# Optimization experiments

Measured on AMD Instinct MI355X. Metric: run time of the kernel, lower is better.

The kernel has to match this reference:

```python
import jax, jax.numpy as jnp
import numpy as np

N_E = 8192      # codebook size
E_DIM = 256     # codebook dim
BETA = 0.25

def setup_inputs() -> dict:
    key = jax.random.key(0)
    k1, k2 = jax.random.split(key)
    z = jax.random.normal(k1, (4, E_DIM, 16, 16, 16), dtype=jnp.float32)
    weight = jax.random.normal(k2, (N_E, E_DIM), dtype=jnp.float32)
    return {"z": z, "weight": weight}

def reference(z, weight):
    # b c d h w -> b d h w c
    z_t = jnp.transpose(z, (0, 2, 3, 4, 1))
    zf = z_t.reshape(-1, E_DIM)                          # [N, e_dim]
    # l2 pairwise distances: |z|^2 + |w|^2 - 2 z.w^T
    d = (jnp.sum(zf * zf, axis=1, keepdims=True)
         + jnp.sum(weight * weight, axis=1)
         - 2.0 * jnp.einsum('bd,nd->bn', zf, weight))    # [N, n_e]
    idx = jnp.argmin(d, axis=1)                          # [N]
    z_q = weight[idx].reshape(z_t.shape)                 # gather lookup
    # perplexity from cluster assignment histogram (avoids dense one-hot)
    counts = jax.ops.segment_sum(jnp.ones_like(idx, dtype=z.dtype), idx,
                                 num_segments=N_E)
    avg_probs = counts / zf.shape[0]
    perplexity = jnp.exp(-jnp.sum(avg_probs * jnp.log(avg_probs + 1e-10)))
    # commitment loss (z_q detached)
    loss = BETA * jnp.mean((jax.lax.stop_gradient(z_q) - z_t) ** 2)
    # straight-through estimator
    z_q_st = z_t + jax.lax.stop_gradient(z_q - z_t)
    out = jnp.transpose(z_q_st, (0, 4, 1, 2, 3))         # b d h w c -> b c d h w
    return out, loss, perplexity, idx
```

## Files before the change

kernel.cpp:

```cpp
#include <hip/hip_runtime.h>
#include <stdint.h>


#define M_TOTAL 16384
#define N_CODES 8192
#define KDIM    256
#define SPATIAL 4096
#define NSPLIT  8
#define CODES_PER_SPLIT  1024
#define CHUNK_CODES      16
#define CHUNKS_PER_SPLIT 64
#define CHUNK_BYTES      9216
#define CHUNK_HALFS      4608

typedef _Float16 v8hf __attribute__((ext_vector_type(8)));
typedef _Float16 v4hf __attribute__((ext_vector_type(4)));
typedef float    v4f  __attribute__((ext_vector_type(4)));

#define WAITCNT_VM9   0x0F79
#define WAITCNT_VM0   0x0F70
#define WAITCNT_LGKM0 0xC07F

__global__ __launch_bounds__(256) void prep_w_kernel(
    const float* __restrict__ w, _Float16* __restrict__ wpk,
    int* __restrict__ counts, double* __restrict__ loss_acc)
{
    const int t = threadIdx.x;
    const int n = blockIdx.x * 4 + (t >> 6);
    const int lane = t & 63;
    v4f v = ((const v4f*)(w + (size_t)n * KDIM))[lane];
    v4hf hv;
    float s = 0.0f;
#pragma unroll
    for (int j = 0; j < 4; j++) {
        float f = v[j];
        s += f * f;
        hv[j] = (_Float16)f;
    }
    const int chunk = n >> 4;
    const int row   = n & 15;
    const int g     = lane >> 1;
    const int gg    = g ^ (n & 7);
    size_t off = (size_t)chunk * CHUNK_HALFS + row * 256 + gg * 8 + (lane & 1) * 4;
    *(v4hf*)(wpk + off) = hv;
#pragma unroll
    for (int o = 32; o >= 1; o >>= 1) s += __shfl_xor(s, o);
    if (lane == 0) {
        float* hwp = (float*)((char*)wpk + (size_t)chunk * CHUNK_BYTES + 8192);
        hwp[row] = 1024.0f - 0.5f * s;
    }
    const int gi = blockIdx.x * 256 + t;
    if (gi < N_CODES) counts[gi] = 0;
    if (gi == 0) *loss_acc = 0.0;
}

__device__ __forceinline__ void top2max_merge(uint32_t& v1, int& i1, uint32_t& v2, int& i2,
                                              uint32_t o1, int oi1, uint32_t o2, int oi2) {
    bool ob = (o1 > v1) || (o1 == v1 && oi1 < i1);
    uint32_t n1v, n2v; int n1i, n2i;
    if (ob) {
        bool t2 = (v1 > o2) || (v1 == o2 && i1 < oi2);
        n1v = o1; n1i = oi1;
        n2v = t2 ? v1 : o2; n2i = t2 ? i1 : oi2;
    } else {
        bool t2 = (o1 > v2) || (o1 == v2 && oi1 < i2);
        n1v = v1; n1i = i1;
        n2v = t2 ? o1 : v2; n2i = t2 ? oi1 : i2;
    }
    v1 = n1v; i1 = n1i; v2 = n2v; i2 = n2i;
}

__global__ __launch_bounds__(64, 2) void gemm_kernel(
    const float* __restrict__ z,
    const _Float16* __restrict__ wpk,
    int4* __restrict__ candbuf)
{
    __shared__ __align__(16) _Float16 lds[2][CHUNK_HALFS];

    const int bid   = blockIdx.x;
    const int split = bid & 7;
    const int rb    = bid >> 3;
    const int i0    = rb * 64;
    const int b     = i0 >> 12;
    const int s0    = i0 & (SPATIAL - 1);
    const int lane  = threadIdx.x;
    const int r     = lane & 15;
    const int q     = lane >> 4;

    const char* wsplit = (const char*)wpk + (size_t)split * CHUNKS_PER_SPLIT * CHUNK_BYTES;
    auto stage = [&](int chunk, int buf) {
        const char* gb = wsplit + (size_t)chunk * CHUNK_BYTES + lane * 16;
        _Float16* lb = &lds[buf][lane * 8];
#pragma unroll
        for (int j = 0; j < 9; j++) {
            __builtin_amdgcn_global_load_lds(
                (const __attribute__((address_space(1))) void*)(gb + j * 1024),
                (__attribute__((address_space(3))) void*)(lb + j * 512), 16, 0, 0);
        }
    };
    stage(0, 0);
    stage(1, 1);

    v8hf a[4][8];
    {
        const float* zb = z + ((size_t)b << 20) + (size_t)(s0 + r);
#pragma unroll
        for (int mt = 0; mt < 4; mt++) {
#pragma unroll
            for (int ks = 0; ks < 8; ks++) {
                const int kbase = ks * 32 + q * 8;
#pragma unroll
                for (int j = 0; j < 8; j++)
                    a[mt][ks][j] = (_Float16)zb[((size_t)(kbase + j) << 12) + mt * 16];
            }
        }
    }

    uint32_t k1[4][4], k2[4][4];
#pragma unroll
    for (int mt = 0; mt < 4; mt++)
#pragma unroll
    for (int g = 0; g < 4; g++) { k1[mt][g] = 0u; k2[mt][g] = 0u; }

    const int swz = r & 7;

    auto body = [&](int it, int buf) {
        const float hwv = *(const float*)((const char*)&lds[buf][0] + 8192 + r * 4);
        v4f acc[4];
#pragma unroll
        for (int mt = 0; mt < 4; mt++) acc[mt] = (v4f){hwv, hwv, hwv, hwv};

        const _Float16* L = &lds[buf][0];
#pragma unroll
        for (int ks = 0; ks < 8; ks++) {
            const int gran = ((ks << 2) | q) ^ swz;
            v8hf bh = *(const v8hf*)(L + r * 256 + (gran << 3));
#pragma unroll
            for (int mt = 0; mt < 4; mt++)
                acc[mt] = __builtin_amdgcn_mfma_f32_16x16x32_f16(a[mt][ks], bh, acc[mt], 0, 0, 0);
        }
        const uint32_t tag = (uint32_t)it;
#pragma unroll
        for (int mt = 0; mt < 4; mt++)
#pragma unroll
        for (int g = 0; g < 4; g++) {
            uint32_t key = (__float_as_uint(acc[mt][g]) & 0xFFFFFFC0u) | tag;
            uint32_t o1 = k1[mt][g], o2 = k2[mt][g];
            uint32_t hi = key > o2 ? key : o2;
            k2[mt][g] = hi < o1 ? hi : o1;
            k1[mt][g] = key > o1 ? key : o1;
        }
    };

#pragma unroll 1
    for (int it = 0; it < CHUNKS_PER_SPLIT - 1; it++) {
        const int buf = it & 1;
        __builtin_amdgcn_s_waitcnt(WAITCNT_VM9);
        body(it, buf);
        __builtin_amdgcn_s_waitcnt(WAITCNT_LGKM0);
        if (it < CHUNKS_PER_SPLIT - 2) stage(it + 2, buf);
    }
    __builtin_amdgcn_s_waitcnt(WAITCNT_VM0);
    body(CHUNKS_PER_SPLIT - 1, (CHUNKS_PER_SPLIT - 1) & 1);

    const int nsbase = split * CODES_PER_SPLIT + r;
#pragma unroll
    for (int mt = 0; mt < 4; mt++) {
#pragma unroll
        for (int g = 0; g < 4; g++) {
            uint32_t K1 = k1[mt][g], K2 = k2[mt][g];
            int n1 = nsbase + (int)((K1 & 63u) << 4);
            int n2 = nsbase + (int)((K2 & 63u) << 4);
#pragma unroll
            for (int off = 1; off < 16; off <<= 1) {
                uint32_t o1 = __shfl_xor(K1, off);
                int     on1 = __shfl_xor(n1, off);
                uint32_t o2 = __shfl_xor(K2, off);
                int     on2 = __shfl_xor(n2, off);
                top2max_merge(K1, n1, K2, n2, o1, on1, o2, on2);
            }
            if (r == 0) {
                const int row = i0 + mt * 16 + q * 4 + g;
                candbuf[(size_t)row * 8 + split] = make_int4((int)K1, n1, (int)K2, n2);
            }
        }
    }
}

__global__ __launch_bounds__(256) void finish_kernel(
    const float* __restrict__ z, const float* __restrict__ weight,
    const int4* __restrict__ candbuf,
    int* __restrict__ counts, double* __restrict__ loss_acc,
    float* __restrict__ out, float* __restrict__ out_idx_f)
{
    __shared__ int4  s_cand[32][8];
    __shared__ float s_zw[32][KDIM + 1];
    __shared__ int   s_fi[32];
    __shared__ double s_loss[4];

    const int i0 = blockIdx.x * 32;
    const int b  = i0 >> 12;
    const int s0 = i0 & (SPATIAL - 1);
    const int t  = threadIdx.x;

    s_cand[t >> 3][t & 7] = candbuf[(size_t)(i0 + (t >> 3)) * 8 + (t & 7)];

    for (int e = t; e < 32 * KDIM; e += 256) {
        const int c = e >> 5, rr = e & 31;
        s_zw[rr][c] = z[((size_t)b << 20) + ((size_t)c << 12) + s0 + rr];
    }
    __syncthreads();

    const int row = t >> 3, seg = t & 7;
    float zs[32];
#pragma unroll
    for (int j = 0; j < 32; j++) zs[j] = s_zw[row][seg * 32 + j];

    float da[16];
    float dmin_a = 3.4e38f;
#pragma unroll
    for (int sp = 0; sp < 8; sp++) {
        int4 c = s_cand[row][sp];
        da[sp * 2]     = 2048.0f - 2.0f * __uint_as_float((uint32_t)c.x & 0xFFFFFFC0u);
        da[sp * 2 + 1] = 2048.0f - 2.0f * __uint_as_float((uint32_t)c.z & 0xFFFFFFC0u);
        dmin_a = fminf(dmin_a, fminf(da[sp * 2], da[sp * 2 + 1]));
    }
    const float cutoff = dmin_a + 0.5f;

    double dbest = 1e300; int nbest = 0x7fffffff;
#pragma unroll 1
    for (int c = 0; c < 16; c++) {
        if (da[c] > cutoff) continue;
        int4 cc = s_cand[row][c >> 1];
        const int n = (c & 1) ? cc.w : cc.y;
        const float* wr = weight + (size_t)n * KDIM + seg * 32;
        double d = 0.0;
#pragma unroll
        for (int j = 0; j < 32; j++) {
            double df = (double)zs[j] - (double)wr[j];
            d += df * df;
        }
#pragma unroll
        for (int o = 1; o < 8; o <<= 1) d += __shfl_xor(d, o);
        if (d < dbest || (d == dbest && n < nbest)) { dbest = d; nbest = n; }
    }

    double lsum = 0.0;
    if (seg == 0) {
        s_fi[row] = nbest;
        out_idx_f[i0 + row] = (float)nbest;
        atomicAdd(&counts[nbest], 1);
        lsum = dbest;
    }
#pragma unroll
    for (int o = 1; o < 64; o <<= 1) lsum += __shfl_xor(lsum, o);
    if ((t & 63) == 0) s_loss[t >> 6] = lsum;
    __syncthreads();
    if (t == 0) atomicAdd(loss_acc, s_loss[0] + s_loss[1] + s_loss[2] + s_loss[3]);

    for (int e = t; e < 32 * KDIM; e += 256) {
        const int rr = e >> 8, c = e & 255;
        s_zw[rr][c] = weight[(size_t)s_fi[rr] * KDIM + c];
    }
    __syncthreads();
    const int m = t & 31, c0 = t >> 5;
    const size_t obase = ((size_t)b << 20) + (size_t)(s0 + m);
    for (int c = c0; c < KDIM; c += 8)
        out[obase + ((size_t)c << 12)] = s_zw[m][c];
}

__global__ void finalize_kernel(const int* __restrict__ counts,
                                const double* __restrict__ loss_acc,
                                float* __restrict__ out_scalars)
{
    const int t = threadIdx.x;
    double s = 0.0;
    for (int n = t; n < N_CODES; n += 256) {
        double p = (double)counts[n] / (double)M_TOTAL;
        s -= p * log(p + 1e-10);
    }
#pragma unroll
    for (int o = 32; o >= 1; o >>= 1) s += __shfl_xor(s, o);
    __shared__ double sds[4];
    if ((t & 63) == 0) sds[t >> 6] = s;
    __syncthreads();
    if (t == 0) {
        double tot = sds[0] + sds[1] + sds[2] + sds[3];
        out_scalars[0] = (float)(0.25 * (*loss_acc) / (double)(M_TOTAL * KDIM));
        out_scalars[1] = (float)exp(tot);
    }
}

extern "C" void kernel_launch(void* const* d_in, const int* in_sizes, int n_in,
                              void* d_out, int out_size, void* d_ws, size_t ws_size,
                              hipStream_t stream) {
    const float* z      = (const float*)d_in[0];
    const float* weight = (const float*)d_in[1];
    float* out = (float*)d_out;

    size_t off = 0;
    auto carve = [&](size_t bytes) {
        void* p = (char*)d_ws + off;
        off += (bytes + 255) & ~(size_t)255;
        return p;
    };
    _Float16* wpk     = (_Float16*)carve((size_t)(N_CODES / CHUNK_CODES) * CHUNK_BYTES);
    int4*     candbuf = (int4*)    carve((size_t)M_TOTAL * 8 * 16);
    int*      counts  = (int*)     carve((size_t)N_CODES * 4);
    double*   lossac  = (double*)  carve(16);

    float* out_scalars = out + (size_t)4 * KDIM * SPATIAL;
    float* out_idx_f   = out_scalars + 2;

    prep_w_kernel<<<dim3(N_CODES / 4), dim3(256), 0, stream>>>(weight, wpk, counts, lossac);
    gemm_kernel<<<dim3(M_TOTAL / 64 * NSPLIT), dim3(64), 0, stream>>>(z, wpk, candbuf);
    finish_kernel<<<dim3(M_TOTAL / 32), dim3(256), 0, stream>>>(
        z, weight, candbuf, counts, lossac, out, out_idx_f);
    finalize_kernel<<<dim3(1), dim3(256), 0, stream>>>(counts, lossac, out_scalars);
}
```

Measured before the change: 209.8 us.

## Share codebook staging across four waves with 4-deep LDS ring and fuse finalize

The GEMM block grows from one wave to four, which share each 32-code fp16 codebook chunk staged in LDS through a 4-buffer ring with barriers. This cuts redundant global-to-LDS traffic per row. The |w|^2 bias now lives in a separate array that is preloaded into LDS. The single-block finalize kernel is folded into finish_kernel through a last-block-done atomic counter, which removes one launch but adds a serial tail in the last block. The grid drops to 512 blocks, so occupancy and latency hiding may change.

```diff
diff --git a/kernel.cpp b/kernel.cpp
--- a/kernel.cpp
+++ b/kernel.cpp
@@ -8,22 +8,19 @@
 #define SPATIAL 4096
 #define NSPLIT  8
 #define CODES_PER_SPLIT  1024
-#define CHUNK_CODES      16
-#define CHUNKS_PER_SPLIT 64
-#define CHUNK_BYTES      9216
-#define CHUNK_HALFS      4608
+#define CHUNK_CODES      32
+#define CHUNKS_PER_SPLIT 32
+#define CHUNK_HALFS      8192
+#define CHUNK_BYTES      16384
 
 typedef _Float16 v8hf __attribute__((ext_vector_type(8)));
 typedef _Float16 v4hf __attribute__((ext_vector_type(4)));
 typedef float    v4f  __attribute__((ext_vector_type(4)));
 
-#define WAITCNT_VM9   0x0F79
-#define WAITCNT_VM0   0x0F70
-#define WAITCNT_LGKM0 0xC07F
-
 __global__ __launch_bounds__(256) void prep_w_kernel(
     const float* __restrict__ w, _Float16* __restrict__ wpk,
-    int* __restrict__ counts, double* __restrict__ loss_acc)
+    float* __restrict__ hw_arr, int* __restrict__ counts,
+    double* __restrict__ loss_acc, int* __restrict__ done_ctr)
 {
     const int t = threadIdx.x;
     const int n = blockIdx.x * 4 + (t >> 6);
@@ -37,21 +34,17 @@
         s += f * f;
         hv[j] = (_Float16)f;
     }
-    const int chunk = n >> 4;
-    const int row   = n & 15;
-    const int g     = lane >> 1;
-    const int gg    = g ^ (n & 7);
+    const int chunk = n >> 5;
+    const int row   = n & 31;
+    const int gg    = (lane >> 1) ^ (n & 7);
     size_t off = (size_t)chunk * CHUNK_HALFS + row * 256 + gg * 8 + (lane & 1) * 4;
     *(v4hf*)(wpk + off) = hv;
 #pragma unroll
     for (int o = 32; o >= 1; o >>= 1) s += __shfl_xor(s, o);
-    if (lane == 0) {
-        float* hwp = (float*)((char*)wpk + (size_t)chunk * CHUNK_BYTES + 8192);
-        hwp[row] = 1024.0f - 0.5f * s;
-    }
+    if (lane == 0) hw_arr[n] = 1024.0f - 0.5f * s;
     const int gi = blockIdx.x * 256 + t;
     if (gi < N_CODES) counts[gi] = 0;
-    if (gi == 0) *loss_acc = 0.0;
+    if (gi == 0) { *loss_acc = 0.0; *done_ctr = 0; }
 }
 
 __device__ __forceinline__ void top2max_merge(uint32_t& v1, int& i1, uint32_t& v2, int& i2,
@@ -70,40 +63,48 @@
     v1 = n1v; i1 = n1i; v2 = n2v; i2 = n2i;
 }
 
-__global__ __launch_bounds__(64, 2) void gemm_kernel(
+__global__ __launch_bounds__(256, 2) void gemm_kernel(
     const float* __restrict__ z,
     const _Float16* __restrict__ wpk,
+    const float* __restrict__ hw_arr,
     int4* __restrict__ candbuf)
 {
-    __shared__ __align__(16) _Float16 lds[2][CHUNK_HALFS];
+    __shared__ __align__(16) _Float16 lds[4][CHUNK_HALFS];
+    __shared__ float hw_lds[CODES_PER_SPLIT];
 
     const int bid   = blockIdx.x;
     const int split = bid & 7;
     const int rb    = bid >> 3;
-    const int i0    = rb * 64;
+    const int i0    = rb * 256;
     const int b     = i0 >> 12;
     const int s0    = i0 & (SPATIAL - 1);
-    const int lane  = threadIdx.x;
+    const int tid   = threadIdx.x;
+    const int wave  = tid >> 6;
+    const int lane  = tid & 63;
     const int r     = lane & 15;
     const int q     = lane >> 4;
 
-    const char* wsplit = (const char*)wpk + (size_t)split * CHUNKS_PER_SPLIT * CHUNK_BYTES;
+    const char* wsplit = (const char*)wpk + (size_t)split * (CODES_PER_SPLIT * KDIM * 2);
     auto stage = [&](int chunk, int buf) {
-        const char* gb = wsplit + (size_t)chunk * CHUNK_BYTES + lane * 16;
-        _Float16* lb = &lds[buf][lane * 8];
-#pragma unroll
-        for (int j = 0; j < 9; j++) {
+        const char* gb = wsplit + (size_t)chunk * CHUNK_BYTES + tid * 16;
+        _Float16* lb = &lds[buf][tid * 8];
+#pragma unroll
+        for (int j = 0; j < 4; j++) {
             __builtin_amdgcn_global_load_lds(
-                (const __attribute__((address_space(1))) void*)(gb + j * 1024),
-                (__attribute__((address_space(3))) void*)(lb + j * 512), 16, 0, 0);
+                (const __attribute__((address_space(1))) void*)(gb + j * 4096),
+                (__attribute__((address_space(3))) void*)(lb + j * 2048), 16, 0, 0);
         }
     };
-    stage(0, 0);
-    stage(1, 1);
+    stage(0, 0); stage(1, 1); stage(2, 2);
+
+    {
+        v4f h = *(const v4f*)(hw_arr + split * CODES_PER_SPLIT + tid * 4);
+        *(v4f*)&hw_lds[tid * 4] = h;
+    }
 
     v8hf a[4][8];
     {
-        const float* zb = z + ((size_t)b << 20) + (size_t)(s0 + r);
+        const float* zb = z + ((size_t)b << 20) + (size_t)(s0 + wave * 64 + r);
 #pragma unroll
         for (int mt = 0; mt < 4; mt++) {
 #pragma unroll
@@ -124,44 +125,59 @@
 
     const int swz = r & 7;
 
+    __syncthreads();
+
     auto body = [&](int it, int buf) {
-        const float hwv = *(const float*)((const char*)&lds[buf][0] + 8192 + r * 4);
-        v4f acc[4];
-#pragma unroll
-        for (int mt = 0; mt < 4; mt++) acc[mt] = (v4f){hwv, hwv, hwv, hwv};
-
+        const float hw0 = hw_lds[it * 32 + r];
+        const float hw1 = hw_lds[it * 32 + 16 + r];
+        v4f acc[4][2];
+#pragma unroll
+        for (int mt = 0; mt < 4; mt++) {
+            acc[mt][0] = (v4f){hw0, hw0, hw0, hw0};
+            acc[mt][1] = (v4f){hw1, hw1, hw1, hw1};
+        }
         const _Float16* L = &lds[buf][0];
 #pragma unroll
-        for (int ks = 0; ks < 8; ks++) {
-            const int gran = ((ks << 2) | q) ^ swz;
-            v8hf bh = *(const v8hf*)(L + r * 256 + (gran << 3));
+        for (int st = 0; st < 2; st++) {
+            const int rowoff = (st * 16 + r) * 256;
+#pragma unroll
+            for (int ks = 0; ks < 8; ks++) {
+                const int gran = ((ks << 2) | q) ^ swz;
+                v8hf bh = *(const v8hf*)(L + rowoff + (gran << 3));
+#pragma unroll
+                for (int mt = 0; mt < 4; mt++)
+                    acc[mt][st] = __builtin_amdgcn_mfma_f32_16x16x32_f16(a[mt][ks], bh, acc[mt][st], 0, 0, 0);
+            }
+        }
+#pragma unroll
+        for (int st = 0; st < 2; st++) {
+            const uint32_t tag = (uint32_t)(it * 2 + st);
 #pragma unroll
             for (int mt = 0; mt < 4; mt++)
-                acc[mt] = __builtin_amdgcn_mfma_f32_16x16x32_f16(a[mt][ks], bh, acc[mt], 0, 0, 0);
-        }
-        const uint32_t tag = (uint32_t)it;
-#pragma unroll
-        for (int mt = 0; mt < 4; mt++)
-#pragma unroll
-        for (int g = 0; g < 4; g++) {
-            uint32_t key = (__float_as_uint(acc[mt][g]) & 0xFFFFFFC0u) | tag;
-            uint32_t o1 = k1[mt][g], o2 = k2[mt][g];
-            uint32_t hi = key > o2 ? key : o2;
-            k2[mt][g] = hi < o1 ? hi : o1;
-            k1[mt][g] = key > o1 ? key : o1;
+#pragma unroll
+            for (int g = 0; g < 4; g++) {
+                uint32_t key = (__float_as_uint(acc[mt][st][g]) & 0xFFFFFFC0u) | tag;
+                uint32_t o1 = k1[mt][g], o2 = k2[mt][g];
+                uint32_t hi = key > o2 ? key : o2;
+                k2[mt][g] = hi < o1 ? hi : o1;
+                k1[mt][g] = key > o1 ? key : o1;
+            }
         }
     };
 
 #pragma unroll 1
-    for (int it = 0; it < CHUNKS_PER_SPLIT - 1; it++) {
-        const int buf = it & 1;
-        __builtin_amdgcn_s_waitcnt(WAITCNT_VM9);
-        body(it, buf);
-        __builtin_amdgcn_s_waitcnt(WAITCNT_LGKM0);
-        if (it < CHUNKS_PER_SPLIT - 2) stage(it + 2, buf);
-    }
-    __builtin_amdgcn_s_waitcnt(WAITCNT_VM0);
-    body(CHUNKS_PER_SPLIT - 1, (CHUNKS_PER_SPLIT - 1) & 1);
+    for (int it = 0; it < CHUNKS_PER_SPLIT - 2; it++) {
+        asm volatile("s_waitcnt vmcnt(8)" ::: "memory");
+        asm volatile("s_barrier" ::: "memory");
+        if (it + 3 < CHUNKS_PER_SPLIT) stage(it + 3, (it + 3) & 3);
+        body(it, it & 3);
+    }
+    asm volatile("s_waitcnt vmcnt(4)" ::: "memory");
+    asm volatile("s_barrier" ::: "memory");
+    body(CHUNKS_PER_SPLIT - 2, (CHUNKS_PER_SPLIT - 2) & 3);
+    asm volatile("s_waitcnt vmcnt(0)" ::: "memory");
+    asm volatile("s_barrier" ::: "memory");
+    body(CHUNKS_PER_SPLIT - 1, (CHUNKS_PER_SPLIT - 1) & 3);
 
     const int nsbase = split * CODES_PER_SPLIT + r;
 #pragma unroll
@@ -180,7 +196,7 @@
                 top2max_merge(K1, n1, K2, n2, o1, on1, o2, on2);
             }
             if (r == 0) {
-                const int row = i0 + mt * 16 + q * 4 + g;
+                const int row = i0 + wave * 64 + mt * 16 + q * 4 + g;
                 candbuf[(size_t)row * 8 + split] = make_int4((int)K1, n1, (int)K2, n2);
             }
         }
@@ -191,12 +207,15 @@
     const float* __restrict__ z, const float* __restrict__ weight,
     const int4* __restrict__ candbuf,
     int* __restrict__ counts, double* __restrict__ loss_acc,
-    float* __restrict__ out, float* __restrict__ out_idx_f)
+    int* __restrict__ done_ctr,
+    float* __restrict__ out, float* __restrict__ out_scalars,
+    float* __restrict__ out_idx_f)
 {
     __shared__ int4  s_cand[32][8];
     __shared__ float s_zw[32][KDIM + 1];
     __shared__ int   s_fi[32];
-    __shared__ double s_loss[4];
+    __shared__ double s_red[4];
+    __shared__ int   s_last;
 
     const int i0 = blockIdx.x * 32;
     const int b  = i0 >> 12;
@@ -254,9 +273,9 @@
     }
 #pragma unroll
     for (int o = 1; o < 64; o <<= 1) lsum += __shfl_xor(lsum, o);
-    if ((t & 63) == 0) s_loss[t >> 6] = lsum;
-    __syncthreads();
-    if (t == 0) atomicAdd(loss_acc, s_loss[0] + s_loss[1] + s_loss[2] + s_loss[3]);
+    if ((t & 63) == 0) s_red[t >> 6] = lsum;
+    __syncthreads();
+    if (t == 0) atomicAdd(loss_acc, s_red[0] + s_red[1] + s_red[2] + s_red[3]);
 
     for (int e = t; e < 32 * KDIM; e += 256) {
         const int rr = e >> 8, c = e & 255;
@@ -267,27 +286,33 @@
     const size_t obase = ((size_t)b << 20) + (size_t)(s0 + m);
     for (int c = c0; c < KDIM; c += 8)
         out[obase + ((size_t)c << 12)] = s_zw[m][c];
-}
-
-__global__ void finalize_kernel(const int* __restrict__ counts,
-                                const double* __restrict__ loss_acc,
-                                float* __restrict__ out_scalars)
-{
-    const int t = threadIdx.x;
-    double s = 0.0;
-    for (int n = t; n < N_CODES; n += 256) {
-        double p = (double)counts[n] / (double)M_TOTAL;
-        s -= p * log(p + 1e-10);
-    }
-#pragma unroll
-    for (int o = 32; o >= 1; o >>= 1) s += __shfl_xor(s, o);
-    __shared__ double sds[4];
-    if ((t & 63) == 0) sds[t >> 6] = s;
-    __syncthreads();
+
     if (t == 0) {
-        double tot = sds[0] + sds[1] + sds[2] + sds[3];
-        out_scalars[0] = (float)(0.25 * (*loss_acc) / (double)(M_TOTAL * KDIM));
-        out_scalars[1] = (float)exp(tot);
+        __threadfence();
+        int old = __hip_atomic_fetch_add(done_ctr, 1, __ATOMIC_ACQ_REL,
+                                         __HIP_MEMORY_SCOPE_AGENT);
+        s_last = (old == (int)gridDim.x - 1);
+    }
+    __syncthreads();
+    if (s_last) {
+        double s = 0.0;
+        for (int n = t; n < N_CODES; n += 256) {
+            int c = __hip_atomic_load(&counts[n], __ATOMIC_RELAXED,
+                                      __HIP_MEMORY_SCOPE_AGENT);
+            double p = (double)c / (double)M_TOTAL;
+            s -= p * log(p + 1e-10);
+        }
+#pragma unroll
+        for (int o = 32; o >= 1; o >>= 1) s += __shfl_xor(s, o);
+        if ((t & 63) == 0) s_red[t >> 6] = s;
+        __syncthreads();
+        if (t == 0) {
+            double tot = s_red[0] + s_red[1] + s_red[2] + s_red[3];
+            double l = __hip_atomic_load(loss_acc, __ATOMIC_RELAXED,
+                                         __HIP_MEMORY_SCOPE_AGENT);
+            out_scalars[0] = (float)(0.25 * l / (double)(M_TOTAL * KDIM));
+            out_scalars[1] = (float)exp(tot);
+        }
     }
 }
 
@@ -304,17 +329,19 @@
         off += (bytes + 255) & ~(size_t)255;
         return p;
     };
-    _Float16* wpk     = (_Float16*)carve((size_t)(N_CODES / CHUNK_CODES) * CHUNK_BYTES);
+    _Float16* wpk     = (_Float16*)carve((size_t)N_CODES * KDIM * 2);
+    float*    hw_arr  = (float*)   carve((size_t)N_CODES * 4);
     int4*     candbuf = (int4*)    carve((size_t)M_TOTAL * 8 * 16);
     int*      counts  = (int*)     carve((size_t)N_CODES * 4);
     double*   lossac  = (double*)  carve(16);
+    int*      donec   = (int*)     carve(16);
 
     float* out_scalars = out + (size_t)4 * KDIM * SPATIAL;
     float* out_idx_f   = out_scalars + 2;
 
-    prep_w_kernel<<<dim3(N_CODES / 4), dim3(256), 0, stream>>>(weight, wpk, counts, lossac);
-    gemm_kernel<<<dim3(M_TOTAL / 64 * NSPLIT), dim3(64), 0, stream>>>(z, wpk, candbuf);
+    prep_w_kernel<<<dim3(N_CODES / 4), dim3(256), 0, stream>>>(
+        weight, wpk, hw_arr, counts, lossac, donec);
+    gemm_kernel<<<dim3(64 * NSPLIT), dim3(256), 0, stream>>>(z, wpk, hw_arr, candbuf);
     finish_kernel<<<dim3(M_TOTAL / 32), dim3(256), 0, stream>>>(
-        z, weight, candbuf, counts, lossac, out, out_idx_f);
-    finalize_kernel<<<dim3(1), dim3(256), 0, stream>>>(counts, lossac, out_scalars);
-}
+        z, weight, candbuf, counts, lossac, donec, out, out_scalars, out_idx_f);
+}
```

New measurement: 239.9 us. 1.14x slower.
